# Kernel optimization log

Measured on AMD Instinct MI355X. Metric: run time of the kernel, lower is better.

Reference implementation:

```python
import jax, jax.numpy as jnp
import numpy as np


def log_g(x):
    # log of g(x) = x + 0.5 for x>=0, sigmoid(x) for x<0
    return jnp.where(x >= 0, jnp.log(jax.nn.relu(x) + 0.5), -jax.nn.softplus(-x))


def setup_inputs() -> dict:
    key = jax.random.key(0)
    k1, k2, k3 = jax.random.split(key, 3)
    bs, seq_len, d_in, H = 4, 4096, 1024, 1024
    scale = 1.0 / np.sqrt(d_in)  # keep pre-activations O(1) so exp() in log-space scan stays finite
    x = jax.random.normal(k1, (bs, seq_len, d_in), dtype=jnp.float32)
    h_0 = jnp.zeros((bs, 1, H), dtype=jnp.float32)
    Wz = jax.random.normal(k2, (H, d_in), dtype=jnp.float32) * scale
    bz = jnp.zeros((H,), dtype=jnp.float32)
    Wh = jax.random.normal(k3, (H, d_in), dtype=jnp.float32) * scale
    bh = jnp.zeros((H,), dtype=jnp.float32)
    return {"x": x, "h_0": h_0, "Wz": Wz, "bz": bz, "Wh": Wh, "bh": bh}


def reference(x, h_0, Wz, bz, Wh, bh):
    bs, seq_len, _ = x.shape
    # gate and candidate pre-activations (two GEMMs)
    k = jnp.einsum("bsd,hd->bsh", x, Wz) + bz          # [bs, S, H]
    log_coeff = -jax.nn.softplus(k)                     # log(1 - z)
    log_z = -jax.nn.softplus(-k)                        # log(z)
    log_tilde_h = log_g(jnp.einsum("bsd,hd->bsh", x, Wh) + bh)
    log_h_0 = log_g(h_0)                                # [bs, 1, H]
    log_value = jnp.concatenate([log_h_0, log_z + log_tilde_h], axis=1)  # [bs, S+1, H]
    # log-space parallel scan: h_t = (1-z_t) h_{t-1} + z_t h~_t
    a_star = jnp.pad(jnp.cumsum(log_coeff, axis=1), ((0, 0), (1, 0), (0, 0)))  # [bs, S+1, H]
    log_h0_plus_b_star = jax.lax.cumlogsumexp(log_value - a_star, axis=1)
    log_prefix = a_star + log_h0_plus_b_star
    return jnp.exp(log_prefix)[:, 1:]                   # [bs, S, H]
```

## Files before the change

### kernel.cpp

```cpp
#include <hip/hip_runtime.h>
#include <cstddef>
#include <cstdint>

#define BSZ   4
#define SEQ   4096
#define DIN   1024
#define HDIM  1024
#define MTOT  (BSZ * SEQ)
#define NELE  ((size_t)MTOT * HDIM)
#define NX    ((size_t)MTOT * DIN)
#define NW    ((size_t)HDIM * DIN)
#define NCH   128
#define CL    (SEQ / NCH)

#define X4 (NX / 4)
#define W4 (NW / 4)

#define GBM 256
#define GBN 128
#define GBK 64
#define NKT (DIN / GBK)

using bf16x8 = __attribute__((ext_vector_type(8))) __bf16;
using f32x4  = __attribute__((ext_vector_type(4))) float;

__device__ __forceinline__ float bf2f(unsigned int u16bits) {
    union { unsigned int i; float f; } v;
    v.i = u16bits << 16;
    return v.f;
}
__device__ __forceinline__ unsigned int pk2(float a, float b) {
    union { float f; unsigned int i; } ua, ub; ua.f = a; ub.f = b;
    return ((ua.i + 0x8000u) >> 16) | ((ub.i + 0x8000u) & 0xffff0000u);
}

__device__ __forceinline__ void gload16(const void* g, void* l) {
    __builtin_amdgcn_global_load_lds(
        (const __attribute__((address_space(1))) unsigned int*)g,
        (__attribute__((address_space(3))) unsigned int*)l, 16, 0, 0);
}

__global__ __launch_bounds__(256) void cvt_bf16(
    const float* __restrict__ x, const float* __restrict__ wz,
    const float* __restrict__ wh, unsigned short* __restrict__ xb,
    unsigned short* __restrict__ zb, unsigned short* __restrict__ hb)
{
    const size_t i = (size_t)blockIdx.x * 256 + threadIdx.x;
    const float4* s; uint4* d; size_t off;
    const size_t xh = X4 / 2, wh4 = W4 / 2;
    if (i < xh)            { s = (const float4*)x;  d = (uint4*)xb; off = i; }
    else if (i < xh + wh4) { s = (const float4*)wz; d = (uint4*)zb; off = i - xh; }
    else                   { s = (const float4*)wh; d = (uint4*)hb; off = i - xh - wh4; }
    const float4 v0 = s[2 * off];
    const float4 v1 = s[2 * off + 1];
    uint4 r;
    r.x = pk2(v0.x, v0.y); r.y = pk2(v0.z, v0.w);
    r.z = pk2(v1.x, v1.y); r.w = pk2(v1.z, v1.w);
    d[off] = r;
}

#define MFMA16(p)                                                              \
    _Pragma("unroll")                                                          \
    for (int i_ = 0; i_ < 2; ++i_) {                                           \
        _Pragma("unroll")                                                      \
        for (int nt_ = 0; nt_ < 2; ++nt_) {                                    \
            accz[2*(p)+i_][nt_] = __builtin_amdgcn_mfma_f32_16x16x32_bf16(     \
                av[i_][0], fz[nt_][0], accz[2*(p)+i_][nt_], 0, 0, 0);          \
            acch[2*(p)+i_][nt_] = __builtin_amdgcn_mfma_f32_16x16x32_bf16(     \
                av[i_][0], fh[nt_][0], acch[2*(p)+i_][nt_], 0, 0, 0);          \
            accz[2*(p)+i_][nt_] = __builtin_amdgcn_mfma_f32_16x16x32_bf16(     \
                av[i_][1], fz[nt_][1], accz[2*(p)+i_][nt_], 0, 0, 0);          \
            acch[2*(p)+i_][nt_] = __builtin_amdgcn_mfma_f32_16x16x32_bf16(     \
                av[i_][1], fh[nt_][1], acch[2*(p)+i_][nt_], 0, 0, 0);          \
        }                                                                      \
    }

#define PHASE(p, STAGE)                                                        \
    {                                                                          \
        bf16x8 av[2][2];                                                       \
        _Pragma("unroll")                                                      \
        for (int i_ = 0; i_ < 2; ++i_) {                                       \
            av[i_][0] = *(const bf16x8*)(bcc + aBase + (2*(p)+i_) * 2048 + k0o);\
            av[i_][1] = *(const bf16x8*)(bcc + aBase + (2*(p)+i_) * 2048 + k1o);\
        }                                                                      \
        STAGE                                                                  \
        __builtin_amdgcn_s_barrier();                                          \
        asm volatile("s_waitcnt lgkmcnt(0)" ::: "memory");                     \
        __builtin_amdgcn_sched_barrier(0);                                     \
        __builtin_amdgcn_s_setprio(1);                                         \
        MFMA16(p)                                                              \
        __builtin_amdgcn_s_setprio(0);                                         \
        __builtin_amdgcn_s_barrier();                                          \
    }

__global__ __launch_bounds__(512, 2) void gemm_act_8ph(
    const unsigned short* __restrict__ xb, const unsigned short* __restrict__ zb,
    const unsigned short* __restrict__ hb, const float* __restrict__ bz,
    const float* __restrict__ bh, unsigned int* __restrict__ ab,
    float* __restrict__ carryA, float* __restrict__ carryB)
{
    __shared__ unsigned short smem[2][32768];

    const int tid  = threadIdx.x;
    const int wid  = tid >> 6;
    const int lane = tid & 63;
    const int lm   = lane & 15;
    const int q    = lane >> 4;
    const int wr   = wid >> 2;
    const int wc   = wid & 3;

    const int bid = blockIdx.x;
    const int swz = (bid & 7) * 64 + (bid >> 3);
    const int ty  = swz >> 3;
    const int tx  = swz & 7;
    const int m0  = ty * GBM;
    const int n0  = tx * GBN;

    const int l8   = lane >> 3;
    const int sl   = lane & 7;
    const int scol = 16 * (sl ^ l8);
    const char* gA = (const char*)xb + ((size_t)(m0 + wid * 32 + l8) * DIN) * 2 + scol;
    const char* gZ = (const char*)zb + ((size_t)(n0 + wid * 16 + l8) * DIN) * 2 + scol;
    const char* gH = (const char*)hb + ((size_t)(n0 + wid * 16 + l8) * DIN) * 2 + scol;
    const int ldsA = wid * 2048;
    const int ldsZ = 16384 + wid * 1024;
    const int ldsH = 24576 + wid * 1024;

    const int sw  = (lm & 7) << 4;
    const int k0o = (q * 16) ^ sw;
    const int k1o = (64 + q * 16) ^ sw;
    const int aBase = (wr * 128 + lm) * 128;
    const int zBase = 32768 + (wc * 32 + lm) * 128;
    const int hBase = 49152 + (wc * 32 + lm) * 128;

    f32x4 accz[8][2], acch[8][2];
#pragma unroll
    for (int mt = 0; mt < 8; ++mt)
#pragma unroll
        for (int nt = 0; nt < 2; ++nt) {
            accz[mt][nt] = (f32x4){0.f, 0.f, 0.f, 0.f};
            acch[mt][nt] = (f32x4){0.f, 0.f, 0.f, 0.f};
        }

    {
        unsigned short* b0 = &smem[0][0];
#pragma unroll
        for (int j = 0; j < 4; ++j) gload16(gA + j * 16384, b0 + ldsA + j * 512);
        gload16(gZ, b0 + ldsZ); gload16(gZ + 16384, b0 + ldsZ + 512);
        gload16(gH, b0 + ldsH); gload16(gH + 16384, b0 + ldsH + 512);
    }

#pragma unroll 2
    for (int kt = 0; kt < NKT; ++kt) {
        const char*     bcc = (const char*)&smem[kt & 1][0];
        unsigned short* bn  = &smem[(kt & 1) ^ 1][0];
        const bool pf = (kt + 1 < NKT);
        const size_t ko = (size_t)(kt + 1) * 128;

        bf16x8 fz[2][2], fh[2][2];

        if (pf) {
#pragma unroll
            for (int j = 0; j < 4; ++j)
                gload16(gA + ko + j * 16384, bn + ldsA + j * 512);
            asm volatile("s_waitcnt vmcnt(4)" ::: "memory");
        } else {
            asm volatile("s_waitcnt vmcnt(0)" ::: "memory");
        }
        __builtin_amdgcn_s_barrier();
#pragma unroll
        for (int nt = 0; nt < 2; ++nt) {
            fz[nt][0] = *(const bf16x8*)(bcc + zBase + nt * 2048 + k0o);
            fz[nt][1] = *(const bf16x8*)(bcc + zBase + nt * 2048 + k1o);
            fh[nt][0] = *(const bf16x8*)(bcc + hBase + nt * 2048 + k0o);
            fh[nt][1] = *(const bf16x8*)(bcc + hBase + nt * 2048 + k1o);
        }
        {
            bf16x8 av[2][2];
#pragma unroll
            for (int i_ = 0; i_ < 2; ++i_) {
                av[i_][0] = *(const bf16x8*)(bcc + aBase + i_ * 2048 + k0o);
                av[i_][1] = *(const bf16x8*)(bcc + aBase + i_ * 2048 + k1o);
            }
            asm volatile("s_waitcnt lgkmcnt(0)" ::: "memory");
            __builtin_amdgcn_sched_barrier(0);
            __builtin_amdgcn_s_setprio(1);
            MFMA16(0)
            __builtin_amdgcn_s_setprio(0);
            __builtin_amdgcn_s_barrier();
        }
        PHASE(1,
            if (pf) {
                gload16(gZ + ko, bn + ldsZ); gload16(gZ + ko + 16384, bn + ldsZ + 512);
                gload16(gH + ko, bn + ldsH); gload16(gH + ko + 16384, bn + ldsH + 512);
            }
        )
        PHASE(2, )
        PHASE(3, )
    }

    const int bi  = m0 >> 12;
    const int cb0 = ((m0 & 4095) >> 5) + wr * 4;

#pragma unroll
    for (int nt = 0; nt < 2; ++nt) {
        const int col = n0 + wc * 32 + nt * 16 + lm;
        const float bzv = bz[col];
        const float bhv = bh[col];
#pragma unroll
        for (int pr = 0; pr < 4; ++pr) {
            float CA = 1.f, CB = 0.f;
#pragma unroll
            for (int mi = 0; mi < 2; ++mi) {
                const int mt   = pr * 2 + mi;
                const int row0 = m0 + wr * 128 + mt * 16 + q * 4;
                float A = 1.f, B = 0.f;
#pragma unroll
                for (int r = 0; r < 4; ++r) {
                    const float kpre = accz[mt][nt][r] + bzv;
                    const float hpre = acch[mt][nt][r] + bhv;
                    const float ez   = __expf(-kpre);
                    const float zv   = 1.0f / (1.0f + ez);
                    const float avv  = ez * zv;
                    const float g    = (hpre >= 0.f) ? (hpre + 0.5f)
                                                     : (1.0f / (1.0f + __expf(-hpre)));
                    const float bv   = zv * g;
                    ab[(size_t)(row0 + r) * HDIM + col] = pk2(avv, bv);
                    A = avv * A;
                    B = fmaf(avv, B, bv);
                }
                float A2 = __shfl_xor(A, 16, 64);
                float B2 = __shfl_xor(B, 16, 64);
                B = (q & 1) ? fmaf(A, B2, B) : fmaf(A2, B, B2);
                A = A * A2;
                A2 = __shfl_xor(A, 32, 64);
                B2 = __shfl_xor(B, 32, 64);
                B = (q & 2) ? fmaf(A, B2, B) : fmaf(A2, B, B2);
                A = A * A2;
                CB = fmaf(A, CB, B);
                CA = A * CA;
            }
            if (q == 0) {
                const int cseq = cb0 + pr;
                const size_t ci = ((size_t)(cseq * BSZ + bi)) * HDIM + col;
                carryA[ci] = CA;
                carryB[ci] = CB;
            }
        }
    }
}

__global__ __launch_bounds__(256) void scan_phaseB(
    const float* __restrict__ h0, const float* __restrict__ carryA,
    const float* __restrict__ carryB, float* __restrict__ hin)
{
    const int h  = blockIdx.x * 256 + threadIdx.x;
    const int bi = blockIdx.y;
    const float v = h0[(size_t)bi * HDIM + h];
    float hr = (v >= 0.0f) ? (v + 0.5f) : (1.0f / (1.0f + __expf(-v)));
    for (int c = 0; c < NCH; ++c) {
        const size_t ci = ((size_t)c * BSZ + bi) * HDIM + h;
        hin[ci] = hr;
        hr = fmaf(carryA[ci], hr, carryB[ci]);
    }
}

__global__ __launch_bounds__(256) void scan_phaseC(
    const unsigned int* __restrict__ ab, const float* __restrict__ hin,
    float* __restrict__ out)
{
    const int c  = blockIdx.x;
    const int bi = blockIdx.y;
    const int h  = threadIdx.x * 4;
    size_t idx = ((size_t)bi * SEQ + (size_t)c * CL) * HDIM + h;
    const size_t ci = ((size_t)c * BSZ + bi) * HDIM + h;
    float4 hr = *(const float4*)&hin[ci];
#pragma unroll 4
    for (int t = 0; t < CL; ++t) {
        const uint4 v = *(const uint4*)&ab[idx];
        hr.x = fmaf(bf2f(v.x & 0xffffu), hr.x, bf2f(v.x >> 16));
        hr.y = fmaf(bf2f(v.y & 0xffffu), hr.y, bf2f(v.y >> 16));
        hr.z = fmaf(bf2f(v.z & 0xffffu), hr.z, bf2f(v.z >> 16));
        hr.w = fmaf(bf2f(v.w & 0xffffu), hr.w, bf2f(v.w >> 16));
        *(float4*)&out[idx] = hr;
        idx += HDIM;
    }
}

extern "C" void kernel_launch(void* const* d_in, const int* in_sizes, int n_in,
                              void* d_out, int out_size, void* d_ws, size_t ws_size,
                              hipStream_t stream)
{
    const float* x  = (const float*)d_in[0];
    const float* h0 = (const float*)d_in[1];
    const float* Wz = (const float*)d_in[2];
    const float* bz = (const float*)d_in[3];
    const float* Wh = (const float*)d_in[4];
    const float* bh = (const float*)d_in[5];
    float* out = (float*)d_out;

    unsigned int*   ab  = (unsigned int*)d_ws;
    unsigned short* xbf = (unsigned short*)(ab + NELE);
    unsigned short* zbf = xbf + NX;
    unsigned short* hbf = zbf + NW;
    float* carryA = (float*)(hbf + NW);
    float* carryB = carryA + (size_t)NCH * BSZ * HDIM;
    float* hin    = carryB + (size_t)NCH * BSZ * HDIM;

    const int cvtBlocks = (int)((X4 + 2 * W4) / 2 / 256);
    cvt_bf16<<<cvtBlocks, 256, 0, stream>>>(x, Wz, Wh, xbf, zbf, hbf);

    dim3 gGrid((MTOT / GBM) * (HDIM / GBN));
    gemm_act_8ph<<<gGrid, 512, 0, stream>>>(xbf, zbf, hbf, bz, bh, ab, carryA, carryB);

    dim3 bGrid(HDIM / 256, BSZ);
    scan_phaseB<<<bGrid, 256, 0, stream>>>(h0, carryA, carryB, hin);

    dim3 cGrid(NCH, BSZ);
    scan_phaseC<<<cGrid, 256, 0, stream>>>(ab, hin, out);
}
```

Baseline: 241.9 us.

## Software-pipeline LDS fragment reads with register double-buffering and one barrier per tile

The GEMM main loop is restructured into two unrolled TILE steps with ping-pong register fragments for A (A0/A1) and for the B operands (Bz/Bh, indexed by stage). The next K-tile's global-to-LDS loads are all issued at the start of a tile. The next tile's first A and B fragments are read from LDS during the last MFMA phase, so each tile needs a single vmcnt wait and barrier instead of barriers around every phase. This removes the per-phase barrier and lgkmcnt stalls so LDS reads overlap MFMA work, at the cost of more live vector registers and a tighter write-after-read margin on the shared buffers.

```diff
diff --git a/kernel.cpp b/kernel.cpp
--- a/kernel.cpp
+++ b/kernel.cpp
@@ -59,38 +59,74 @@
     d[off] = r;
 }
 
-#define MFMA16(p)                                                              \
+#define SBAR  __builtin_amdgcn_sched_barrier(0)
+#define PRIO1 __builtin_amdgcn_s_setprio(1)
+#define PRIO0 __builtin_amdgcn_s_setprio(0)
+
+#define MFMA1(acc, va, vb) \
+    acc = __builtin_amdgcn_mfma_f32_16x16x32_bf16(va, vb, acc, 0, 0, 0)
+
+#define MFMA_PAIR(P, AV, S)                                                    \
     _Pragma("unroll")                                                          \
     for (int i_ = 0; i_ < 2; ++i_) {                                           \
         _Pragma("unroll")                                                      \
         for (int nt_ = 0; nt_ < 2; ++nt_) {                                    \
-            accz[2*(p)+i_][nt_] = __builtin_amdgcn_mfma_f32_16x16x32_bf16(     \
-                av[i_][0], fz[nt_][0], accz[2*(p)+i_][nt_], 0, 0, 0);          \
-            acch[2*(p)+i_][nt_] = __builtin_amdgcn_mfma_f32_16x16x32_bf16(     \
-                av[i_][0], fh[nt_][0], acch[2*(p)+i_][nt_], 0, 0, 0);          \
-            accz[2*(p)+i_][nt_] = __builtin_amdgcn_mfma_f32_16x16x32_bf16(     \
-                av[i_][1], fz[nt_][1], accz[2*(p)+i_][nt_], 0, 0, 0);          \
-            acch[2*(p)+i_][nt_] = __builtin_amdgcn_mfma_f32_16x16x32_bf16(     \
-                av[i_][1], fh[nt_][1], acch[2*(p)+i_][nt_], 0, 0, 0);          \
+            MFMA1(accz[2*(P)+i_][nt_], AV[i_][0], Bz[S][nt_][0]);              \
+            MFMA1(acch[2*(P)+i_][nt_], AV[i_][0], Bh[S][nt_][0]);              \
+            MFMA1(accz[2*(P)+i_][nt_], AV[i_][1], Bz[S][nt_][1]);              \
+            MFMA1(acch[2*(P)+i_][nt_], AV[i_][1], Bh[S][nt_][1]);              \
         }                                                                      \
     }
 
-#define PHASE(p, STAGE)                                                        \
+#define READ_A(AV, MTP, B)                                                     \
+    AV[0][0] = *(const bf16x8*)((B) + aBase + (2*(MTP)+0)*2048 + k0o);         \
+    AV[0][1] = *(const bf16x8*)((B) + aBase + (2*(MTP)+0)*2048 + k1o);         \
+    AV[1][0] = *(const bf16x8*)((B) + aBase + (2*(MTP)+1)*2048 + k0o);         \
+    AV[1][1] = *(const bf16x8*)((B) + aBase + (2*(MTP)+1)*2048 + k1o);
+
+#define READ_B_HALF(SS, NT, B)                                                 \
+    Bz[SS][NT][0] = *(const bf16x8*)((B) + zBase + (NT)*2048 + k0o);           \
+    Bz[SS][NT][1] = *(const bf16x8*)((B) + zBase + (NT)*2048 + k1o);           \
+    Bh[SS][NT][0] = *(const bf16x8*)((B) + hBase + (NT)*2048 + k0o);           \
+    Bh[SS][NT][1] = *(const bf16x8*)((B) + hBase + (NT)*2048 + k1o);
+
+#define STAGE8(BN, KO)                                                         \
+    gload16(gA + (KO),          (BN) + ldsA);                                  \
+    gload16(gA + (KO) + 16384,  (BN) + ldsA + 512);                            \
+    gload16(gA + (KO) + 32768,  (BN) + ldsA + 1024);                           \
+    gload16(gA + (KO) + 49152,  (BN) + ldsA + 1536);                           \
+    gload16(gZ + (KO),          (BN) + ldsZ);                                  \
+    gload16(gZ + (KO) + 16384,  (BN) + ldsZ + 512);                            \
+    gload16(gH + (KO),          (BN) + ldsH);                                  \
+    gload16(gH + (KO) + 16384,  (BN) + ldsH + 512);
+
+#define TILE(KT, S)                                                            \
     {                                                                          \
-        bf16x8 av[2][2];                                                       \
-        _Pragma("unroll")                                                      \
-        for (int i_ = 0; i_ < 2; ++i_) {                                       \
-            av[i_][0] = *(const bf16x8*)(bcc + aBase + (2*(p)+i_) * 2048 + k0o);\
-            av[i_][1] = *(const bf16x8*)(bcc + aBase + (2*(p)+i_) * 2048 + k1o);\
+        const int ktv = (KT);                                                  \
+        const char*     bcc = (const char*)&smem[S][0];                        \
+        unsigned short* bn  = &smem[(S) ^ 1][0];                               \
+        const char*     bnc = (const char*)bn;                                 \
+        const bool pf = (ktv + 1 < NKT);                                       \
+        const size_t ko = (size_t)(ktv + 1) * 128;                             \
+                                                                       \
+        if (pf) { STAGE8(bn, ko) }                                             \
+        READ_A(A1, 1, bcc)                                                     \
+        PRIO1; MFMA_PAIR(0, A0, S) PRIO0; SBAR;                                \
+                                                                       \
+        READ_A(A0, 2, bcc)                                                     \
+        PRIO1; MFMA_PAIR(1, A1, S) PRIO0; SBAR;                                \
+                                                                       \
+        READ_A(A1, 3, bcc)                                                     \
+        PRIO1; MFMA_PAIR(2, A0, S) PRIO0; SBAR;                                \
+                \
+        if (pf) {                                                              \
+            asm volatile("s_waitcnt vmcnt(0)" ::: "memory");                   \
+            __builtin_amdgcn_s_barrier();                                      \
+            READ_B_HALF((S) ^ 1, 0, bnc)                                       \
+            READ_A(A0, 0, bnc)                                                 \
         }                                                                      \
-        STAGE                                                                  \
-        __builtin_amdgcn_s_barrier();                                          \
-        asm volatile("s_waitcnt lgkmcnt(0)" ::: "memory");                     \
-        __builtin_amdgcn_sched_barrier(0);                                     \
-        __builtin_amdgcn_s_setprio(1);                                         \
-        MFMA16(p)                                                              \
-        __builtin_amdgcn_s_setprio(0);                                         \
-        __builtin_amdgcn_s_barrier();                                          \
+        PRIO1; MFMA_PAIR(3, A1, S) PRIO0; SBAR;                                \
+        if (pf) { READ_B_HALF((S) ^ 1, 1, bnc) }                               \
     }
 
 __global__ __launch_bounds__(512, 2) void gemm_act_8ph(
@@ -142,61 +178,23 @@
             acch[mt][nt] = (f32x4){0.f, 0.f, 0.f, 0.f};
         }
 
+    bf16x8 A0[2][2], A1[2][2];
+    bf16x8 Bz[2][2][2], Bh[2][2][2];
+
     {
         unsigned short* b0 = &smem[0][0];
-#pragma unroll
-        for (int j = 0; j < 4; ++j) gload16(gA + j * 16384, b0 + ldsA + j * 512);
-        gload16(gZ, b0 + ldsZ); gload16(gZ + 16384, b0 + ldsZ + 512);
-        gload16(gH, b0 + ldsH); gload16(gH + 16384, b0 + ldsH + 512);
-    }
-
-#pragma unroll 2
-    for (int kt = 0; kt < NKT; ++kt) {
-        const char*     bcc = (const char*)&smem[kt & 1][0];
-        unsigned short* bn  = &smem[(kt & 1) ^ 1][0];
-        const bool pf = (kt + 1 < NKT);
-        const size_t ko = (size_t)(kt + 1) * 128;
-
-        bf16x8 fz[2][2], fh[2][2];
-
-        if (pf) {
-#pragma unroll
-            for (int j = 0; j < 4; ++j)
-                gload16(gA + ko + j * 16384, bn + ldsA + j * 512);
-            asm volatile("s_waitcnt vmcnt(4)" ::: "memory");
-        } else {
-            asm volatile("s_waitcnt vmcnt(0)" ::: "memory");
-        }
+        const char*     b0c = (const char*)b0;
+        STAGE8(b0, 0)
+        asm volatile("s_waitcnt vmcnt(0)" ::: "memory");
         __builtin_amdgcn_s_barrier();
-#pragma unroll
-        for (int nt = 0; nt < 2; ++nt) {
-            fz[nt][0] = *(const bf16x8*)(bcc + zBase + nt * 2048 + k0o);
-            fz[nt][1] = *(const bf16x8*)(bcc + zBase + nt * 2048 + k1o);
-            fh[nt][0] = *(const bf16x8*)(bcc + hBase + nt * 2048 + k0o);
-            fh[nt][1] = *(const bf16x8*)(bcc + hBase + nt * 2048 + k1o);
-        }
-        {
-            bf16x8 av[2][2];
-#pragma unroll
-            for (int i_ = 0; i_ < 2; ++i_) {
-                av[i_][0] = *(const bf16x8*)(bcc + aBase + i_ * 2048 + k0o);
-                av[i_][1] = *(const bf16x8*)(bcc + aBase + i_ * 2048 + k1o);
-            }
-            asm volatile("s_waitcnt lgkmcnt(0)" ::: "memory");
-            __builtin_amdgcn_sched_barrier(0);
-            __builtin_amdgcn_s_setprio(1);
-            MFMA16(0)
-            __builtin_amdgcn_s_setprio(0);
-            __builtin_amdgcn_s_barrier();
-        }
-        PHASE(1,
-            if (pf) {
-                gload16(gZ + ko, bn + ldsZ); gload16(gZ + ko + 16384, bn + ldsZ + 512);
-                gload16(gH + ko, bn + ldsH); gload16(gH + ko + 16384, bn + ldsH + 512);
-            }
-        )
-        PHASE(2, )
-        PHASE(3, )
+        READ_B_HALF(0, 0, b0c)
+        READ_B_HALF(0, 1, b0c)
+        READ_A(A0, 0, b0c)
+    }
+
+    for (int kt = 0; kt < NKT; kt += 2) {
+        TILE(kt, 0)
+        TILE(kt + 1, 1)
     }
 
     const int bi  = m0 >> 12;
```

New measurement: 240.1 us. No clear change (-0.7%).
